# Performance work log

Hardware: AMD Instinct MI355X
Metric: run time of the kernel (lower is better)

## Reference

```python
import jax, jax.numpy as jnp
import numpy as np

N = 100000
H = 128
F_IN = 32
F_OUT = 16
NUM_GRAPHS = 64
NEG_SLOPE = 0.2


def setup_inputs() -> dict:
    key = jax.random.key(0)
    ks = jax.random.split(key, 16)
    inp = {
        'x': jax.random.normal(ks[0], (N, F_IN), dtype=jnp.float32),
        'edge_index': jax.random.randint(ks[1], (2, 1000000), 0, N, dtype=jnp.int32),
        'subgraph_edge_index': jax.random.randint(ks[2], (2, 1000000), 0, N, dtype=jnp.int32),
        'node_subnode_index': jax.random.randint(ks[3], (2, 200000), 0, N, dtype=jnp.int32),
        'subnode_node_index': jax.random.randint(ks[4], (2, 200000), 0, N, dtype=jnp.int32),
        'ground_node': jnp.arange(40000, dtype=jnp.int32),
        'subgraph_batch_index': jax.random.randint(ks[5], (60000,), 0, NUM_GRAPHS, dtype=jnp.int32),
        'batch_idx': jax.random.randint(ks[6], (40000,), 0, NUM_GRAPHS, dtype=jnp.int32),
    }
    s_in = 1.0 / np.sqrt(F_IN)
    s_h = 1.0 / np.sqrt(H)
    inp['emb_W'] = jax.random.uniform(ks[7], (F_IN, H), jnp.float32, -s_in, s_in)
    inp['emb_b'] = jax.random.uniform(ks[8], (H,), jnp.float32, -s_in, s_in)
    # 4 GATv2 layers (depth=1): lin_l, lin_r, att, bias per layer
    inp['Wl'] = jax.random.uniform(ks[9], (4, H, H), jnp.float32, -s_h, s_h)
    inp['Wr'] = jax.random.uniform(ks[10], (4, H, H), jnp.float32, -s_h, s_h)
    inp['att'] = jax.random.uniform(ks[11], (4, H), jnp.float32, -s_h, s_h)
    inp['bias'] = jax.random.uniform(ks[12], (4, H), jnp.float32, -s_h, s_h)
    inp['out_W'] = jax.random.uniform(ks[13], (H, F_OUT), jnp.float32, -s_h, s_h)
    inp['out_b'] = jax.random.uniform(ks[14], (F_OUT,), jnp.float32, -s_h, s_h)
    return inp


def _gatv2(x, ei, Wl, Wr, att, b):
    # add self loops (PyG GATv2Conv default add_self_loops=True)
    loops = jnp.broadcast_to(jnp.arange(N, dtype=ei.dtype)[None, :], (2, N))
    ei = jnp.concatenate([ei, loops], axis=1)
    src, dst = ei[0], ei[1]
    xl = x @ Wl  # source transform [N,H]
    xr = x @ Wr  # target transform [N,H]
    e = jax.nn.leaky_relu(xl[src] + xr[dst], NEG_SLOPE) @ att  # [E]
    m = jax.ops.segment_max(e, dst, num_segments=N)
    p = jnp.exp(e - m[dst])
    s = jax.ops.segment_sum(p, dst, num_segments=N)
    alpha = p / s[dst]
    out = jax.ops.segment_sum(alpha[:, None] * xl[src], dst, num_segments=N)
    return out + b


def reference(x, edge_index, subgraph_edge_index, node_subnode_index,
              subnode_node_index, ground_node, subgraph_batch_index, batch_idx,
              emb_W, emb_b, Wl, Wr, att, bias, out_W, out_b):
    h = x @ emb_W + emb_b
    eis = (edge_index, node_subnode_index, subgraph_edge_index, subnode_node_index)
    for i, ei in enumerate(eis):
        h = _gatv2(h, ei, Wl[i], Wr[i], att[i], bias[i])
    # global_add_pool over ground nodes
    pooled = jax.ops.segment_sum(h[ground_node], batch_idx, num_segments=NUM_GRAPHS)
    return pooled @ out_W + out_b
```

## Files before the change

### kernel.cpp

```cpp
#include <hip/hip_runtime.h>
#include <cstddef>


typedef __attribute__((ext_vector_type(8))) short bf16x8;
typedef __attribute__((ext_vector_type(4))) float f32x4;

#define NSH   10
#define CHUNK 8192
#define POOLP 256

__device__ __forceinline__ unsigned short f2bf(float f) {
  unsigned int u = __float_as_uint(f);
  u += 0x7fffu + ((u >> 16) & 1u);
  return (unsigned short)(u >> 16);
}
__device__ __forceinline__ float bf2f(short s) {
  return __uint_as_float(((unsigned int)(unsigned short)s) << 16);
}

__device__ __forceinline__ int lds_excl_scan(int* a, int len, int* aux, int tid)
{
  int g = (len + 255) >> 8;
  int lo = tid * g;
  int s = 0;
  for (int i = 0; i < g; ++i) { int idx = lo + i; if (idx < len) s += a[idx]; }
  aux[tid] = s;
  __syncthreads();
  for (int d = 1; d < 256; d <<= 1) {
    int v = (tid >= d) ? aux[tid - d] : 0;
    __syncthreads();
    aux[tid] += v;
    __syncthreads();
  }
  int run = aux[tid] - s;
  for (int i = 0; i < g; ++i) {
    int idx = lo + i;
    if (idx < len) { int t = a[idx]; a[idx] = run; run += t; }
  }
  int total = aux[255];
  __syncthreads();
  return total;
}

__device__ __forceinline__ void resolve_item(
    int id, int t1, int t2, int t3, int t4, int n,
    const int* s0, const int* s1, const int* s2, const int* s3,
    const int* d0, const int* d1, const int* d2, const int* d3,
    int& l, int& s, int& d, bool need_src)
{
  if (id < t4) {
    const int *sp, *dp; int e;
    if      (id < t1) { l = 0; e = id;      sp = s0; dp = d0; }
    else if (id < t2) { l = 1; e = id - t1; sp = s1; dp = d1; }
    else if (id < t3) { l = 2; e = id - t2; sp = s2; dp = d2; }
    else              { l = 3; e = id - t3; sp = s3; dp = d3; }
    d = dp[e];
    s = need_src ? sp[e] : 0;
  } else {
    int k = id - t4;
    l = (k >= 3 * n) ? 3 : (k >= 2 * n) ? 2 : (k >= n) ? 1 : 0;
    s = k - l * n; d = s;
  }
}

__global__ __launch_bounds__(256) void setup_kernel(
    const float* __restrict__ Wl, const float* __restrict__ Wr,
    const float* __restrict__ embW,
    unsigned short* __restrict__ packB, unsigned short* __restrict__ packE,
    int* __restrict__ offs4, int n, int e0, int e1, int e2, int e3)
{
  int id = blockIdx.x * 256 + threadIdx.x;
  if (id < 131072) {
    int j    = id & 7;
    int lane = (id >> 3) & 63;
    int kt   = (id >> 9) & 3;
    int ct   = (id >> 11) & 15;
    int l    = id >> 15;
    int k    = kt * 32 + (lane >> 4) * 8 + j;
    int col  = ct * 16 + (lane & 15);
    float v = (ct < 8) ? Wl[(size_t)l * 16384 + k * 128 + col]
                       : Wr[(size_t)l * 16384 + k * 128 + (col - 128)];
    packB[id] = f2bf(v);
  }
  int pe = id - 131072;
  if (pe >= 0 && pe < 4096) {
    int j    = pe & 7;
    int lane = (pe >> 3) & 63;
    int ct   = pe >> 9;
    int k    = (lane >> 4) * 8 + j;
    int col  = ct * 16 + (lane & 15);
    packE[pe] = f2bf(embW[k * 128 + col]);
  }
  int q = pe - 4096;
  if (q >= 0 && q < 4) {
    int El = (q == 0) ? e0 : (q == 1) ? e1 : (q == 2) ? e2 : e3;
    offs4[(size_t)q * (n + 1) + n] = El + n;
  }
}

__global__ __launch_bounds__(256) void embed_mfma_kernel(
    const float* __restrict__ x, const unsigned short* __restrict__ packE,
    const float* __restrict__ b, unsigned short* __restrict__ hb, int n)
{
  const int wave = threadIdx.x >> 6;
  const int lane = threadIdx.x & 63;
  const int rlan = lane & 15;
  const int kgrp = lane >> 4;

  bf16x8 Bf[8];
#pragma unroll
  for (int ct = 0; ct < 8; ++ct)
    Bf[ct] = *(const bf16x8*)(packE + ((size_t)ct * 64 + lane) * 8);
  float bv[8];
#pragma unroll
  for (int ct = 0; ct < 8; ++ct) bv[ct] = b[ct * 16 + rlan];

  const float4* __restrict__ x4 = (const float4*)x;
  const int ntiles = (n + 15) / 16;
  for (int tile = blockIdx.x * 4 + wave; tile < ntiles; tile += gridDim.x * 4) {
    int r = tile * 16 + rlan;
    if (r >= n) r = n - 1;
    float4 a0 = x4[(size_t)r * 8 + kgrp * 2];
    float4 a1 = x4[(size_t)r * 8 + kgrp * 2 + 1];
    bf16x8 Af;
    Af[0] = (short)f2bf(a0.x); Af[1] = (short)f2bf(a0.y);
    Af[2] = (short)f2bf(a0.z); Af[3] = (short)f2bf(a0.w);
    Af[4] = (short)f2bf(a1.x); Af[5] = (short)f2bf(a1.y);
    Af[6] = (short)f2bf(a1.z); Af[7] = (short)f2bf(a1.w);

    f32x4 acc[8];
#pragma unroll
    for (int ct = 0; ct < 8; ++ct) {
      acc[ct] = (f32x4){0.f, 0.f, 0.f, 0.f};
      acc[ct] = __builtin_amdgcn_mfma_f32_16x16x32_bf16(Af, Bf[ct], acc[ct], 0, 0, 0);
    }
    int rowb = tile * 16 + kgrp * 4;
#pragma unroll
    for (int ct = 0; ct < 8; ++ct) {
      int col = ct * 16 + rlan;
#pragma unroll
      for (int rr = 0; rr < 4; ++rr)
        if (rowb + rr < n)
          hb[(size_t)(rowb + rr) * 128 + col] = f2bf(acc[ct][rr] + bv[ct]);
    }
  }
}

__global__ __launch_bounds__(256) void gemm_mfma_kernel(
    const unsigned short* __restrict__ hb,
    const unsigned short* __restrict__ packB,
    unsigned short* __restrict__ xlb, unsigned short* __restrict__ xrb, int n)
{
  const int wave = threadIdx.x >> 6;
  const int lane = threadIdx.x & 63;
  const int rlan = lane & 15;
  const int kgrp = lane >> 4;

  bf16x8 Bf[4][4];
#pragma unroll
  for (int ct = 0; ct < 4; ++ct)
#pragma unroll
    for (int kt = 0; kt < 4; ++kt)
      Bf[ct][kt] = *(const bf16x8*)(packB +
          ((((size_t)(wave * 4 + ct)) * 4 + kt) * 64 + lane) * 8);

  unsigned short* __restrict__ outp = (wave < 2) ? xlb : xrb;
  const int colbase = (wave & 1) * 64;

  const int ntiles = (n + 31) / 32;
  for (int tile = blockIdx.x; tile < ntiles; tile += gridDim.x) {
    const int row0 = tile * 32;
    bf16x8 Af[2][4];
#pragma unroll
    for (int rt = 0; rt < 2; ++rt) {
      int r = row0 + rt * 16 + rlan;
      if (r >= n) r = n - 1;
      const unsigned short* ap = hb + (size_t)r * 128 + kgrp * 8;
#pragma unroll
      for (int kt = 0; kt < 4; ++kt)
        Af[rt][kt] = *(const bf16x8*)(ap + kt * 32);
    }
    f32x4 acc[2][4];
#pragma unroll
    for (int rt = 0; rt < 2; ++rt)
#pragma unroll
      for (int ct = 0; ct < 4; ++ct)
        acc[rt][ct] = (f32x4){0.f, 0.f, 0.f, 0.f};
#pragma unroll
    for (int kt = 0; kt < 4; ++kt)
#pragma unroll
      for (int rt = 0; rt < 2; ++rt)
#pragma unroll
        for (int ct = 0; ct < 4; ++ct)
          acc[rt][ct] = __builtin_amdgcn_mfma_f32_16x16x32_bf16(
              Af[rt][kt], Bf[ct][kt], acc[rt][ct], 0, 0, 0);
#pragma unroll
    for (int rt = 0; rt < 2; ++rt) {
      int rowb = row0 + rt * 16 + kgrp * 4;
#pragma unroll
      for (int ct = 0; ct < 4; ++ct) {
        int col = colbase + ct * 16 + rlan;
        size_t base = (size_t)rowb * 128 + col;
#pragma unroll
        for (int r = 0; r < 4; ++r)
          if (rowb + r < n) outp[base + (size_t)r * 128] = f2bf(acc[rt][ct][r]);
      }
    }
  }
}

__global__ __launch_bounds__(256) void hist_kernel(
    const int* __restrict__ d0, const int* __restrict__ d1,
    const int* __restrict__ d2, const int* __restrict__ d3,
    int e0, int e1, int e2, int e3, int n, int nbk, int NB, int nitems,
    int* __restrict__ mat)
{
  __shared__ int hist[512];
  int tid = threadIdx.x, c = blockIdx.x;
  for (int i = tid; i < NB; i += 256) hist[i] = 0;
  __syncthreads();
  int t1 = e0, t2 = t1 + e1, t3 = t2 + e2, t4 = t3 + e3;
  int base = c * CHUNK;
#pragma unroll
  for (int k = 0; k < CHUNK / 256; ++k) {
    int id = base + k * 256 + tid;
    if (id < nitems) {
      int l, s, d;
      resolve_item(id, t1, t2, t3, t4, n,
                   nullptr, nullptr, nullptr, nullptr, d0, d1, d2, d3,
                   l, s, d, false);
      atomicAdd(&hist[l * nbk + (d >> NSH)], 1);
    }
  }
  __syncthreads();
  for (int i = tid; i < NB; i += 256) mat[(size_t)c * NB + i] = hist[i];
}

__global__ __launch_bounds__(256) void colscan_a_kernel(
    int* __restrict__ mat, int nchunk, int NB, int* __restrict__ colsum)
{
  __shared__ int col[512];
  __shared__ int aux[256];
  int gb = blockIdx.x, tid = threadIdx.x;
  for (int i = tid; i < nchunk; i += 256) col[i] = mat[(size_t)i * NB + gb];
  __syncthreads();
  int tot = lds_excl_scan(col, nchunk, aux, tid);
  for (int i = tid; i < nchunk; i += 256) mat[(size_t)i * NB + gb] = col[i];
  if (tid == 0) colsum[gb] = tot;
}

__global__ __launch_bounds__(256) void colscan_b_kernel(
    const int* __restrict__ colsum, int NB, int* __restrict__ colscan)
{
  __shared__ int buf[512];
  __shared__ int aux[256];
  int tid = threadIdx.x;
  for (int i = tid; i < NB; i += 256) buf[i] = colsum[i];
  __syncthreads();
  int tot = lds_excl_scan(buf, NB, aux, tid);
  for (int i = tid; i < NB; i += 256) colscan[i] = buf[i];
  if (tid == 0) colscan[NB] = tot;
}

__global__ __launch_bounds__(256) void scatter_kernel(
    const int* __restrict__ s0, const int* __restrict__ s1,
    const int* __restrict__ s2, const int* __restrict__ s3,
    const int* __restrict__ d0, const int* __restrict__ d1,
    const int* __restrict__ d2, const int* __restrict__ d3,
    int e0, int e1, int e2, int e3, int n, int nbk, int NB, int nitems,
    const int* __restrict__ mat, const int* __restrict__ colscan,
    int* __restrict__ staging)
{
  __shared__ int lbuf[CHUNK];
  __shared__ int hist[512];
  __shared__ int cur[512];
  __shared__ int basex[512];
  __shared__ int aux[256];
  int tid = threadIdx.x, c = blockIdx.x;
  for (int i = tid; i < NB; i += 256) hist[i] = 0;
  __syncthreads();
  int t1 = e0, t2 = t1 + e1, t3 = t2 + e2, t4 = t3 + e3;
  int base = c * CHUNK;
#pragma unroll
  for (int k = 0; k < CHUNK / 256; ++k) {
    int id = base + k * 256 + tid;
    if (id < nitems) {
      int l, s, d;
      resolve_item(id, t1, t2, t3, t4, n,
                   nullptr, nullptr, nullptr, nullptr, d0, d1, d2, d3,
                   l, s, d, false);
      atomicAdd(&hist[l * nbk + (d >> NSH)], 1);
    }
  }
  __syncthreads();
  lds_excl_scan(hist, NB, aux, tid);
  for (int i = tid; i < NB; i += 256) {
    cur[i]   = hist[i];
    basex[i] = colscan[i] + mat[(size_t)c * NB + i];
  }
  __syncthreads();
#pragma unroll
  for (int k = 0; k < CHUNK / 256; ++k) {
    int id = base + k * 256 + tid;
    if (id < nitems) {
      int l, s, d;
      resolve_item(id, t1, t2, t3, t4, n,
                   s0, s1, s2, s3, d0, d1, d2, d3, l, s, d, true);
      int gb = l * nbk + (d >> NSH);
      int p = atomicAdd(&cur[gb], 1);
      lbuf[p] = s | ((d & ((1 << NSH) - 1)) << 17);
    }
  }
  __syncthreads();
  int wave = tid >> 6, lane = tid & 63;
  for (int gb = wave; gb < NB; gb += 4) {
    int st = hist[gb], en = cur[gb];
    int gbase = basex[gb];
    for (int j = lane; j < en - st; j += 64)
      staging[gbase + j] = lbuf[st + j];
  }
}

__global__ __launch_bounds__(256) void finalize_kernel(
    const int* __restrict__ staging, const int* __restrict__ colscan,
    int* __restrict__ offs4, int* __restrict__ csr4, int n, int nbk,
    int cb0, int cb1, int cb2, int cb3)
{
  __shared__ int cnt[1 << NSH];
  __shared__ int pos[1 << NSH];
  __shared__ int aux[256];
  int gb = blockIdx.x, tid = threadIdx.x;
  int l = gb / nbk, b = gb % nbk;
  int beg = colscan[gb], end = colscan[gb + 1];
  int node0 = b << NSH;
  int ncount = n - node0; if (ncount > (1 << NSH)) ncount = 1 << NSH;
  int cbl = (l == 0) ? cb0 : (l == 1) ? cb1 : (l == 2) ? cb2 : cb3;

  for (int i = tid; i < (1 << NSH); i += 256) cnt[i] = 0;
  __syncthreads();
  for (int t = beg + tid; t < end; t += 256)
    atomicAdd(&cnt[staging[t] >> 17], 1);
  __syncthreads();
  lds_excl_scan(cnt, 1 << NSH, aux, tid);
  for (int i = tid; i < (1 << NSH); i += 256) {
    if (i < ncount)
      offs4[(size_t)l * (n + 1) + node0 + i] = beg + cnt[i] - cbl;
    pos[i] = cnt[i];
  }
  __syncthreads();
  for (int t = beg + tid; t < end; t += 256) {
    int e = staging[t];
    int p = atomicAdd(&pos[e >> 17], 1);
    csr4[beg + p] = e & 0x1FFFF;
  }
}

__global__ __launch_bounds__(256) void gat_dst_kernel(
    const unsigned short* __restrict__ xlb,
    const unsigned short* __restrict__ xrb,
    const int* __restrict__ offs, const int* __restrict__ csr,
    const float* __restrict__ att, const float* __restrict__ bias,
    float* __restrict__ hout_f, unsigned short* __restrict__ hout_b, int n)
{
  int wid  = (blockIdx.x * 256 + threadIdx.x) >> 6;
  int lane = threadIdx.x & 63;
  if (wid >= n) return;
  int g = lane >> 4;
  int c = lane & 15;

  bf16x8 xr8 = *(const bf16x8*)(xrb + (size_t)wid * 128 + c * 8);
  float xrv[8], a[8];
#pragma unroll
  for (int k = 0; k < 8; ++k) { xrv[k] = bf2f(xr8[k]); a[k] = att[c * 8 + k]; }

  int beg = offs[wid], end = offs[wid + 1];
  float ssum = 0.f, acc[8];
#pragma unroll
  for (int k = 0; k < 8; ++k) acc[k] = 0.f;

  for (int j0 = beg; j0 < end; j0 += 4) {
    int j  = j0 + g;
    int jj = (j < end) ? j : end - 1;
    int s  = csr[jj];
    bf16x8 xs8 = *(const bf16x8*)(xlb + (size_t)s * 128 + c * 8);
    float xs[8];
#pragma unroll
    for (int k = 0; k < 8; ++k) xs[k] = bf2f(xs8[k]);
    float part = 0.f;
#pragma unroll
    for (int k = 0; k < 8; ++k) {
      float t = xs[k] + xrv[k];
      t = (t > 0.f) ? t : 0.2f * t;
      part = fmaf(t, a[k], part);
    }
    part += __shfl_xor(part, 1, 64);
    part += __shfl_xor(part, 2, 64);
    part += __shfl_xor(part, 4, 64);
    part += __shfl_xor(part, 8, 64);
    float p = (j < end) ? __expf(part) : 0.f;
    ssum += p;
#pragma unroll
    for (int k = 0; k < 8; ++k) acc[k] = fmaf(p, xs[k], acc[k]);
  }
#pragma unroll
  for (int k = 0; k < 8; ++k) {
    acc[k] += __shfl_xor(acc[k], 16, 64);
    acc[k] += __shfl_xor(acc[k], 32, 64);
  }
  ssum += __shfl_xor(ssum, 16, 64);
  ssum += __shfl_xor(ssum, 32, 64);

  float inv = 1.0f / ssum;
  float o[8];
#pragma unroll
  for (int k = 0; k < 8; ++k) o[k] = fmaf(acc[k], inv, bias[c * 8 + k]);

  if (lane < 16) {
    if (hout_f) {
      float4 v0 = make_float4(o[0], o[1], o[2], o[3]);
      float4 v1 = make_float4(o[4], o[5], o[6], o[7]);
      *(float4*)(hout_f + (size_t)wid * 128 + c * 8)     = v0;
      *(float4*)(hout_f + (size_t)wid * 128 + c * 8 + 4) = v1;
    } else {
      bf16x8 ob;
#pragma unroll
      for (int k = 0; k < 8; ++k) ob[k] = (short)f2bf(o[k]);
      *(bf16x8*)(hout_b + (size_t)wid * 128 + c * 8) = ob;
    }
  }
}

__global__ __launch_bounds__(256) void pool_partial_kernel(
    const float* __restrict__ h, const int* __restrict__ gnode,
    const int* __restrict__ bidx, float* __restrict__ partial, int ng)
{
  __shared__ float acc[64 * 128];
  int tid = threadIdx.x;
  for (int t = tid; t < 64 * 128; t += 256) acc[t] = 0.f;
  __syncthreads();
  int col = tid & 127, half = tid >> 7;
  for (int nd = blockIdx.x * 2 + half; nd < ng; nd += gridDim.x * 2) {
    int row = gnode[nd];
    int g   = bidx[nd];
    atomicAdd(&acc[g * 128 + col], h[(size_t)row * 128 + col]);
  }
  __syncthreads();
  float* out = partial + (size_t)blockIdx.x * 8192;
  for (int t = tid; t < 64 * 128; t += 256) out[t] = acc[t];
}

__global__ __launch_bounds__(256) void pool_reduce_kernel(
    const float* __restrict__ partial, float* __restrict__ pooled)
{
  int i = blockIdx.x * 256 + threadIdx.x;
  float s = 0.f;
  for (int p = 0; p < POOLP; ++p) s += partial[(size_t)p * 8192 + i];
  pooled[i] = s;
}

__global__ __launch_bounds__(256) void out_gemm_kernel(
    const float* __restrict__ pooled, const float* __restrict__ W,
    const float* __restrict__ b, float* __restrict__ out)
{
  int id = blockIdx.x * 256 + threadIdx.x;
  if (id >= 64 * 16) return;
  int g = id >> 4, f = id & 15;
  float acc = b[f];
#pragma unroll
  for (int k = 0; k < 128; ++k)
    acc += pooled[g * 128 + k] * W[k * 16 + f];
  out[id] = acc;
}

extern "C" void kernel_launch(void* const* d_in, const int* in_sizes, int n_in,
                              void* d_out, int out_size, void* d_ws, size_t ws_size,
                              hipStream_t stream)
{
  const float* x    = (const float*)d_in[0];
  const int* ei0    = (const int*)d_in[1];
  const int* ei_sg  = (const int*)d_in[2];
  const int* ei_ns  = (const int*)d_in[3];
  const int* ei_sn  = (const int*)d_in[4];
  const int* gnode  = (const int*)d_in[5];
  const int* bidx   = (const int*)d_in[7];
  const float* embW = (const float*)d_in[8];
  const float* embB = (const float*)d_in[9];
  const float* Wl   = (const float*)d_in[10];
  const float* Wr   = (const float*)d_in[11];
  const float* att  = (const float*)d_in[12];
  const float* bias = (const float*)d_in[13];
  const float* outW = (const float*)d_in[14];
  const float* outB = (const float*)d_in[15];

  const int n  = in_sizes[0] / 32;
  const int ng = in_sizes[5];

  const int  E_arr[4] = { in_sizes[1] / 2, in_sizes[3] / 2,
                          in_sizes[2] / 2, in_sizes[4] / 2 };
  const int* eptr[4]  = { ei0, ei_ns, ei_sg, ei_sn };
  const int E_tot  = E_arr[0] + E_arr[1] + E_arr[2] + E_arr[3];
  const int nitems = E_tot + 4 * n;
  const int nbk    = (n + (1 << NSH) - 1) >> NSH;
  const int NB     = 4 * nbk;
  const int nchunk = (nitems + CHUNK - 1) / CHUNK;
  int cb[4];
  cb[0] = 0;
  for (int i = 1; i < 4; ++i) cb[i] = cb[i - 1] + E_arr[i - 1] + n;

  char* ws = (char*)d_ws;
  size_t off = 0;
  auto alloc = [&](size_t bytes) -> void* {
    void* p = ws + off;
    off = (off + bytes + 255) & ~(size_t)255;
    return p;
  };
  float*          h      = (float*)alloc((size_t)n * 128 * sizeof(float));
  unsigned short* hb     = (unsigned short*)alloc((size_t)n * 128 * sizeof(unsigned short));
  unsigned short* xlb    = (unsigned short*)alloc((size_t)n * 128 * sizeof(unsigned short));
  unsigned short* xrb    = (unsigned short*)alloc((size_t)n * 128 * sizeof(unsigned short));
  int*            offs4  = (int*)alloc((size_t)4 * (n + 1) * sizeof(int));
  int*            mat    = (int*)alloc((size_t)nchunk * NB * sizeof(int));
  int*            colsum = (int*)alloc((size_t)NB * sizeof(int));
  int*            colscan= (int*)alloc((size_t)(NB + 1) * sizeof(int));
  int*            staging= (int*)alloc((size_t)nitems * sizeof(int));
  int*            csr4   = (int*)alloc((size_t)nitems * sizeof(int));
  unsigned short* packB  = (unsigned short*)alloc(131072 * sizeof(unsigned short));
  unsigned short* packE  = (unsigned short*)alloc(4096 * sizeof(unsigned short));
  float*          partial= (float*)alloc((size_t)POOLP * 8192 * sizeof(float));
  float*          pooled = (float*)alloc(64 * 128 * sizeof(float));
  (void)ws_size; (void)n_in; (void)out_size;

  const int* D[4] = { eptr[0] + E_arr[0], eptr[1] + E_arr[1],
                      eptr[2] + E_arr[2], eptr[3] + E_arr[3] };

  int setup_items = 131072 + 4096 + 4;
  setup_kernel<<<(setup_items + 255) / 256, 256, 0, stream>>>(
      Wl, Wr, embW, packB, packE, offs4, n,
      E_arr[0], E_arr[1], E_arr[2], E_arr[3]);

  const int ntile16 = (n + 15) / 16;
  embed_mfma_kernel<<<(ntile16 + 3) / 4, 256, 0, stream>>>(
      x, packE, embB, hb, n);

  hist_kernel<<<nchunk, 256, 0, stream>>>(
      D[0], D[1], D[2], D[3], E_arr[0], E_arr[1], E_arr[2], E_arr[3],
      n, nbk, NB, nitems, mat);
  colscan_a_kernel<<<NB, 256, 0, stream>>>(mat, nchunk, NB, colsum);
  colscan_b_kernel<<<1, 256, 0, stream>>>(colsum, NB, colscan);
  scatter_kernel<<<nchunk, 256, 0, stream>>>(
      eptr[0], eptr[1], eptr[2], eptr[3], D[0], D[1], D[2], D[3],
      E_arr[0], E_arr[1], E_arr[2], E_arr[3], n, nbk, NB, nitems,
      mat, colscan, staging);
  finalize_kernel<<<NB, 256, 0, stream>>>(
      staging, colscan, offs4, csr4, n, nbk, cb[0], cb[1], cb[2], cb[3]);

  const int gemm_grid = ((n + 31) / 32 + 1) / 2;
  for (int l = 0; l < 4; ++l) {
    gemm_mfma_kernel<<<gemm_grid, 256, 0, stream>>>(
        hb, packB + (size_t)l * 32768, xlb, xrb, n);
    gat_dst_kernel<<<((size_t)n * 64 + 255) / 256, 256, 0, stream>>>(
        xlb, xrb, offs4 + (size_t)l * (n + 1), csr4 + cb[l],
        att + (size_t)l * 128, bias + (size_t)l * 128,
        (l == 3) ? h : nullptr, (l < 3) ? hb : nullptr, n);
  }

  pool_partial_kernel<<<POOLP, 256, 0, stream>>>(h, gnode, bidx, partial, ng);
  pool_reduce_kernel<<<8192 / 256, 256, 0, stream>>>(partial, pooled);
  out_gemm_kernel<<<4, 256, 0, stream>>>(pooled, outW, outB, (float*)d_out);
}
```

Before: 591.1 us.

## Reuse chunk histograms in scatter, truncate bf16 output, pack GAT arithmetic

```diff
diff --git a/kernel.cpp b/kernel.cpp
--- a/kernel.cpp
+++ b/kernel.cpp
@@ -14,8 +14,15 @@
   u += 0x7fffu + ((u >> 16) & 1u);
   return (unsigned short)(u >> 16);
 }
+__device__ __forceinline__ unsigned short f2bf_rtz(float f) {
+  return (unsigned short)(__float_as_uint(f) >> 16);
+}
 __device__ __forceinline__ float bf2f(short s) {
   return __uint_as_float(((unsigned int)(unsigned short)s) << 16);
+}
+__device__ __forceinline__ float2 unpk(unsigned int u) {
+  return make_float2(__uint_as_float(u << 16),
+                     __uint_as_float(u & 0xFFFF0000u));
 }
 
 __device__ __forceinline__ int lds_excl_scan(int* a, int len, int* aux, int tid)
@@ -203,7 +210,8 @@
         size_t base = (size_t)rowb * 128 + col;
 #pragma unroll
         for (int r = 0; r < 4; ++r)
-          if (rowb + r < n) outp[base + (size_t)r * 128] = f2bf(acc[rt][ct][r]);
+          if (rowb + r < n)
+            outp[base + (size_t)r * 128] = f2bf_rtz(acc[rt][ct][r]);
       }
     }
   }
@@ -237,7 +245,8 @@
 }
 
 __global__ __launch_bounds__(256) void colscan_a_kernel(
-    int* __restrict__ mat, int nchunk, int NB, int* __restrict__ colsum)
+    const int* __restrict__ mat, int* __restrict__ pfx,
+    int nchunk, int NB, int* __restrict__ colsum)
 {
   __shared__ int col[512];
   __shared__ int aux[256];
@@ -245,7 +254,7 @@
   for (int i = tid; i < nchunk; i += 256) col[i] = mat[(size_t)i * NB + gb];
   __syncthreads();
   int tot = lds_excl_scan(col, nchunk, aux, tid);
-  for (int i = tid; i < nchunk; i += 256) mat[(size_t)i * NB + gb] = col[i];
+  for (int i = tid; i < nchunk; i += 256) pfx[(size_t)i * NB + gb] = col[i];
   if (tid == 0) colsum[gb] = tot;
 }
 
@@ -268,8 +277,8 @@
     const int* __restrict__ d0, const int* __restrict__ d1,
     const int* __restrict__ d2, const int* __restrict__ d3,
     int e0, int e1, int e2, int e3, int n, int nbk, int NB, int nitems,
-    const int* __restrict__ mat, const int* __restrict__ colscan,
-    int* __restrict__ staging)
+    const int* __restrict__ mat, const int* __restrict__ pfx,
+    const int* __restrict__ colscan, int* __restrict__ staging)
 {
   __shared__ int lbuf[CHUNK];
   __shared__ int hist[512];
@@ -277,28 +286,16 @@
   __shared__ int basex[512];
   __shared__ int aux[256];
   int tid = threadIdx.x, c = blockIdx.x;
-  for (int i = tid; i < NB; i += 256) hist[i] = 0;
-  __syncthreads();
-  int t1 = e0, t2 = t1 + e1, t3 = t2 + e2, t4 = t3 + e3;
-  int base = c * CHUNK;
-#pragma unroll
-  for (int k = 0; k < CHUNK / 256; ++k) {
-    int id = base + k * 256 + tid;
-    if (id < nitems) {
-      int l, s, d;
-      resolve_item(id, t1, t2, t3, t4, n,
-                   nullptr, nullptr, nullptr, nullptr, d0, d1, d2, d3,
-                   l, s, d, false);
-      atomicAdd(&hist[l * nbk + (d >> NSH)], 1);
-    }
-  }
+  for (int i = tid; i < NB; i += 256) hist[i] = mat[(size_t)c * NB + i];
   __syncthreads();
   lds_excl_scan(hist, NB, aux, tid);
   for (int i = tid; i < NB; i += 256) {
     cur[i]   = hist[i];
-    basex[i] = colscan[i] + mat[(size_t)c * NB + i];
-  }
-  __syncthreads();
+    basex[i] = colscan[i] + pfx[(size_t)c * NB + i];
+  }
+  __syncthreads();
+  int t1 = e0, t2 = t1 + e1, t3 = t2 + e2, t4 = t3 + e3;
+  int base = c * CHUNK;
 #pragma unroll
   for (int k = 0; k < CHUNK / 256; ++k) {
     int id = base + k * 256 + tid;
@@ -368,52 +365,60 @@
   int g = lane >> 4;
   int c = lane & 15;
 
-  bf16x8 xr8 = *(const bf16x8*)(xrb + (size_t)wid * 128 + c * 8);
-  float xrv[8], a[8];
-#pragma unroll
-  for (int k = 0; k < 8; ++k) { xrv[k] = bf2f(xr8[k]); a[k] = att[c * 8 + k]; }
+  uint4 xru = *(const uint4*)(xrb + (size_t)wid * 128 + c * 8);
+  float2 xr0 = unpk(xru.x), xr1 = unpk(xru.y);
+  float2 xr2 = unpk(xru.z), xr3 = unpk(xru.w);
+  const float2* att2 = (const float2*)att + c * 4;
+  float2 a0 = att2[0], a1 = att2[1], a2 = att2[2], a3 = att2[3];
 
   int beg = offs[wid], end = offs[wid + 1];
-  float ssum = 0.f, acc[8];
-#pragma unroll
-  for (int k = 0; k < 8; ++k) acc[k] = 0.f;
+  float ssum = 0.f;
+  float2 ac0 = {0.f, 0.f}, ac1 = {0.f, 0.f};
+  float2 ac2 = {0.f, 0.f}, ac3 = {0.f, 0.f};
 
   for (int j0 = beg; j0 < end; j0 += 4) {
     int j  = j0 + g;
     int jj = (j < end) ? j : end - 1;
     int s  = csr[jj];
-    bf16x8 xs8 = *(const bf16x8*)(xlb + (size_t)s * 128 + c * 8);
-    float xs[8];
-#pragma unroll
-    for (int k = 0; k < 8; ++k) xs[k] = bf2f(xs8[k]);
-    float part = 0.f;
-#pragma unroll
-    for (int k = 0; k < 8; ++k) {
-      float t = xs[k] + xrv[k];
-      t = (t > 0.f) ? t : 0.2f * t;
-      part = fmaf(t, a[k], part);
-    }
+    uint4 xu = *(const uint4*)(xlb + (size_t)s * 128 + c * 8);
+    float2 xs0 = unpk(xu.x), xs1 = unpk(xu.y);
+    float2 xs2 = unpk(xu.z), xs3 = unpk(xu.w);
+    float2 t0 = {xs0.x + xr0.x, xs0.y + xr0.y};
+    float2 t1 = {xs1.x + xr1.x, xs1.y + xr1.y};
+    float2 t2 = {xs2.x + xr2.x, xs2.y + xr2.y};
+    float2 t3 = {xs3.x + xr3.x, xs3.y + xr3.y};
+    t0.x = fmaxf(t0.x, 0.2f * t0.x); t0.y = fmaxf(t0.y, 0.2f * t0.y);
+    t1.x = fmaxf(t1.x, 0.2f * t1.x); t1.y = fmaxf(t1.y, 0.2f * t1.y);
+    t2.x = fmaxf(t2.x, 0.2f * t2.x); t2.y = fmaxf(t2.y, 0.2f * t2.y);
+    t3.x = fmaxf(t3.x, 0.2f * t3.x); t3.y = fmaxf(t3.y, 0.2f * t3.y);
+    float2 pp = {t0.x * a0.x, t0.y * a0.y};
+    pp.x = fmaf(t1.x, a1.x, pp.x); pp.y = fmaf(t1.y, a1.y, pp.y);
+    pp.x = fmaf(t2.x, a2.x, pp.x); pp.y = fmaf(t2.y, a2.y, pp.y);
+    pp.x = fmaf(t3.x, a3.x, pp.x); pp.y = fmaf(t3.y, a3.y, pp.y);
+    float part = pp.x + pp.y;
     part += __shfl_xor(part, 1, 64);
     part += __shfl_xor(part, 2, 64);
     part += __shfl_xor(part, 4, 64);
     part += __shfl_xor(part, 8, 64);
     float p = (j < end) ? __expf(part) : 0.f;
     ssum += p;
-#pragma unroll
-    for (int k = 0; k < 8; ++k) acc[k] = fmaf(p, xs[k], acc[k]);
-  }
+    ac0.x = fmaf(p, xs0.x, ac0.x); ac0.y = fmaf(p, xs0.y, ac0.y);
+    ac1.x = fmaf(p, xs1.x, ac1.x); ac1.y = fmaf(p, xs1.y, ac1.y);
+    ac2.x = fmaf(p, xs2.x, ac2.x); ac2.y = fmaf(p, xs2.y, ac2.y);
+    ac3.x = fmaf(p, xs3.x, ac3.x); ac3.y = fmaf(p, xs3.y, ac3.y);
+  }
+  float o[8] = {ac0.x, ac0.y, ac1.x, ac1.y, ac2.x, ac2.y, ac3.x, ac3.y};
 #pragma unroll
   for (int k = 0; k < 8; ++k) {
-    acc[k] += __shfl_xor(acc[k], 16, 64);
-    acc[k] += __shfl_xor(acc[k], 32, 64);
+    o[k] += __shfl_xor(o[k], 16, 64);
+    o[k] += __shfl_xor(o[k], 32, 64);
   }
   ssum += __shfl_xor(ssum, 16, 64);
   ssum += __shfl_xor(ssum, 32, 64);
 
   float inv = 1.0f / ssum;
-  float o[8];
-#pragma unroll
-  for (int k = 0; k < 8; ++k) o[k] = fmaf(acc[k], inv, bias[c * 8 + k]);
+#pragma unroll
+  for (int k = 0; k < 8; ++k) o[k] = fmaf(o[k], inv, bias[c * 8 + k]);
 
   if (lane < 16) {
     if (hout_f) {
@@ -520,6 +525,7 @@
   unsigned short* xrb    = (unsigned short*)alloc((size_t)n * 128 * sizeof(unsigned short));
   int*            offs4  = (int*)alloc((size_t)4 * (n + 1) * sizeof(int));
   int*            mat    = (int*)alloc((size_t)nchunk * NB * sizeof(int));
+  int*            pfx    = (int*)alloc((size_t)nchunk * NB * sizeof(int));
   int*            colsum = (int*)alloc((size_t)NB * sizeof(int));
   int*            colscan= (int*)alloc((size_t)(NB + 1) * sizeof(int));
   int*            staging= (int*)alloc((size_t)nitems * sizeof(int));
@@ -545,12 +551,12 @@
   hist_kernel<<<nchunk, 256, 0, stream>>>(
       D[0], D[1], D[2], D[3], E_arr[0], E_arr[1], E_arr[2], E_arr[3],
       n, nbk, NB, nitems, mat);
-  colscan_a_kernel<<<NB, 256, 0, stream>>>(mat, nchunk, NB, colsum);
+  colscan_a_kernel<<<NB, 256, 0, stream>>>(mat, pfx, nchunk, NB, colsum);
   colscan_b_kernel<<<1, 256, 0, stream>>>(colsum, NB, colscan);
   scatter_kernel<<<nchunk, 256, 0, stream>>>(
       eptr[0], eptr[1], eptr[2], eptr[3], D[0], D[1], D[2], D[3],
       E_arr[0], E_arr[1], E_arr[2], E_arr[3], n, nbk, NB, nitems,
-      mat, colscan, staging);
+      mat, pfx, colscan, staging);
   finalize_kernel<<<NB, 256, 0, stream>>>(
       staging, colscan, offs4, csr4, n, nbk, cb[0], cb[1], cb[2], cb[3]);
 
```

New measurement: 572.3 us. -3.2%, faster.
